# Optimization experiments

Measured on AMD Instinct MI355X. Metric: run time of the kernel, lower is better.

The kernel has to match this reference:

```python
import jax, jax.numpy as jnp
import numpy as np

R = 128            # coarse grid resolution (hash-grid domain)
SCALE = 2          # scale_factor
VS_COARSE = 1.0    # coarse voxel size
VS_FINE = VS_COARSE / SCALE
N_IN = 400_000
C = 32

# 8 trilinear corner offsets, fixed
CORNERS = np.stack(np.meshgrid([0, 1], [0, 1], [0, 1], indexing='ij'), -1).reshape(-1, 3)


def setup_inputs() -> dict:
    key = jax.random.key(0)
    k1, k2 = jax.random.split(key)
    coarse_coords = jax.random.randint(k1, (N_IN, 3), 0, R, dtype=jnp.int32)
    feat = jax.random.normal(k2, (N_IN, C), dtype=jnp.float32)
    # fine grid = subdivided coarse grid: each coarse voxel -> SCALE^3 children
    offs = jnp.stack(
        jnp.meshgrid(jnp.arange(SCALE), jnp.arange(SCALE), jnp.arange(SCALE), indexing='ij'),
        -1).reshape(-1, 3).astype(jnp.int32)  # [8,3]
    fine_coords = (coarse_coords[:, None, :] * SCALE + offs[None]).reshape(-1, 3)  # [8*N_IN,3]
    return {"feat": feat, "coarse_coords": coarse_coords, "fine_coords": fine_coords}


def reference(feat, coarse_coords, fine_coords):
    """Trilinear upsample: sample coarse sparse-voxel features at fine voxel centers.
    Emulates in_grid.sample_trilinear(out_grid.grid_to_world(active_coords), feat).
    Hash-grid lookup is emulated with a dense index volume; missing neighbors
    contribute zero feature (standard sparse-grid convention).
    """
    n_in = feat.shape[0]
    # build coord -> row index volume (stand-in for the voxel hash map)
    table = -jnp.ones((R, R, R), jnp.int32)
    table = table.at[coarse_coords[:, 0], coarse_coords[:, 1], coarse_coords[:, 2]].set(
        jnp.arange(n_in, dtype=jnp.int32))
    # fine voxel centers in world space (centers at (ijk+0.5)*voxel_size)
    out_pos = (fine_coords.astype(jnp.float32) + 0.5) * VS_FINE          # [M,3]
    # continuous coarse-grid coords; coarse centers at (i+0.5)*VS_COARSE
    g = out_pos / VS_COARSE - 0.5                                        # [M,3]
    base = jnp.floor(g)
    frac = g - base                                                      # [M,3]
    corners = jnp.asarray(CORNERS, jnp.int32)                            # [8,3]
    cc = base.astype(jnp.int32)[:, None, :] + corners[None]              # [M,8,3]
    inb = jnp.all((cc >= 0) & (cc < R), axis=-1)                         # [M,8]
    ccc = jnp.clip(cc, 0, R - 1)
    idx = table[ccc[..., 0], ccc[..., 1], ccc[..., 2]]                   # [M,8]
    valid = inb & (idx >= 0)
    # trilinear weights: prod over xyz of frac or (1-frac)
    w3 = jnp.where(corners[None].astype(jnp.float32) > 0,
                   frac[:, None, :], 1.0 - frac[:, None, :])             # [M,8,3]
    w = jnp.prod(w3, axis=-1) * valid.astype(jnp.float32)                # [M,8]
    f = feat[jnp.clip(idx, 0, n_in - 1)]                                 # [M,8,C]
    return jnp.einsum('mk,mkc->mc', w, f)                                # [M,C]
```

## Files before the change

kernel.cpp:

```cpp
#include <hip/hip_runtime.h>


#define R 128
#define TABLE_ELEMS (R * R * R)

typedef float f32x4 __attribute__((ext_vector_type(4)));

__global__ void build_table_kernel(const int* __restrict__ coarse,
                                   int* __restrict__ table, int n) {
    int i = blockIdx.x * blockDim.x + threadIdx.x;
    if (i >= n) return;
    int x = coarse[i * 3 + 0];
    int y = coarse[i * 3 + 1];
    int z = coarse[i * 3 + 2];
    atomicMax(&table[(x * R + y) * R + z], i);
}

__global__ void __launch_bounds__(256)
upsample_kernel(const f32x4* __restrict__ feat4,
                const int* __restrict__ coarse,
                const int* __restrict__ table,
                f32x4* __restrict__ out4,
                int n_in) {
    __shared__ f32x4 sm[4][27 * 8];

    int wib  = threadIdx.x >> 6;
    int lane = threadIdx.x & 63;
    int vi   = blockIdx.x * 4 + wib;
    vi = __builtin_amdgcn_readfirstlane(vi);
    if (vi >= n_in) return;

    int cx = coarse[vi * 3 + 0];
    int cy = coarse[vi * 3 + 1];
    int cz = coarse[vi * 3 + 2];

    int myidx = -1;
    if (lane < 27) {
        int dx  = lane / 9;
        int rem = lane - dx * 9;
        int dy  = rem / 3;
        int dz  = rem - dy * 3;
        int x = cx + dx - 1, y = cy + dy - 1, z = cz + dz - 1;
        if ((unsigned)x < (unsigned)R && (unsigned)y < (unsigned)R &&
            (unsigned)z < (unsigned)R)
            myidx = table[(x * R + y) * R + z];
    }
    unsigned long long vmask = __ballot(myidx >= 0);

    int g = lane >> 3;
    int part = lane & 7;
    f32x4* smw = sm[wib];
#pragma unroll
    for (int r = 0; r < 4; ++r) {
        int nb  = r * 8 + g;
        int idx = __shfl(myidx, nb);
        if (idx >= 0)
            smw[nb * 8 + part] = feat4[(size_t)idx * 8 + part];
    }
    asm volatile("s_waitcnt lgkmcnt(0)" ::: "memory");
    __builtin_amdgcn_sched_barrier(0);

    int ox = (g >> 2) & 1, oy = (g >> 1) & 1, oz = g & 1;
    float wx0 = 0.25f + 0.5f * (float)ox, wx1 = 0.75f - 0.5f * (float)ox;
    float wy0 = 0.25f + 0.5f * (float)oy, wy1 = 0.75f - 0.5f * (float)oy;
    float wz0 = 0.25f + 0.5f * (float)oz, wz1 = 0.75f - 0.5f * (float)oz;

    f32x4 acc = (f32x4)(0.f);
#pragma unroll
    for (int k = 0; k < 8; ++k) {
        int kx = (k >> 2) & 1, ky = (k >> 1) & 1, kz = k & 1;
        int nb = (ox + kx) * 9 + (oy + ky) * 3 + (oz + kz);
        if ((vmask >> nb) & 1ull) {
            float w = (kx ? wx1 : wx0) * (ky ? wy1 : wy0) * (kz ? wz1 : wz0);
            f32x4 f = smw[nb * 8 + part];
            acc += w * f;
        }
    }

    __builtin_nontemporal_store(acc, &out4[(size_t)vi * 64 + lane]);
}

extern "C" void kernel_launch(void* const* d_in, const int* in_sizes, int n_in_arrs,
                              void* d_out, int out_size, void* d_ws, size_t ws_size,
                              hipStream_t stream) {
    const float* feat = (const float*)d_in[0];
    const int* coarse = (const int*)d_in[1];

    int n_in = in_sizes[1] / 3;
    int* table = (int*)d_ws;

    hipMemsetAsync(table, 0xFF, (size_t)TABLE_ELEMS * sizeof(int), stream);

    build_table_kernel<<<(n_in + 255) / 256, 256, 0, stream>>>(coarse, table, n_in);

    int nblocks = (n_in + 3) / 4;
    upsample_kernel<<<nblocks, 256, 0, stream>>>(
        (const f32x4*)feat, coarse, table, (f32x4*)d_out, n_in);
}
```

Baseline: 580.7 us.

## Reorder voxel processing by spatial 8^3 bucket for gather locality

Adds a counting sort of coarse voxels into 4096 spatial buckets (count, single-block scan, atomic scatter) and has the upsample kernel process voxels in that permuted order. Neighbouring waves then touch nearby table entries and shared neighbour features, which is meant to improve cache hit rates on the random gathers. The cost is two extra kernel launches, contended atomics on bucket counters, and output writes that become scattered rather than sequential.

```diff
diff --git a/kernel.cpp b/kernel.cpp
--- a/kernel.cpp
+++ b/kernel.cpp
@@ -3,32 +3,77 @@
 
 #define R 128
 #define TABLE_ELEMS (R * R * R)
+#define NBUCKET 4096
 
 typedef float f32x4 __attribute__((ext_vector_type(4)));
 
+__device__ __forceinline__ int bucket_of(int x, int y, int z) {
+    return ((x >> 3) << 8) | ((y >> 3) << 4) | (z >> 3);
+}
+
 __global__ void build_table_kernel(const int* __restrict__ coarse,
-                                   int* __restrict__ table, int n) {
+                                   int* __restrict__ table,
+                                   int* __restrict__ counts, int n) {
     int i = blockIdx.x * blockDim.x + threadIdx.x;
     if (i >= n) return;
     int x = coarse[i * 3 + 0];
     int y = coarse[i * 3 + 1];
     int z = coarse[i * 3 + 2];
     atomicMax(&table[(x * R + y) * R + z], i);
+    atomicAdd(&counts[bucket_of(x, y, z)], 1);
+}
+
+__global__ void __launch_bounds__(256)
+scan_kernel(const int* __restrict__ counts, int* __restrict__ offs) {
+    __shared__ int part[256];
+    int t = threadIdx.x;
+    int local[16];
+    int s = 0;
+#pragma unroll
+    for (int k = 0; k < 16; ++k) {
+        local[k] = s;
+        s += counts[t * 16 + k];
+    }
+    part[t] = s;
+    __syncthreads();
+    for (int d = 1; d < 256; d <<= 1) {
+        int v = (t >= d) ? part[t - d] : 0;
+        __syncthreads();
+        part[t] += v;
+        __syncthreads();
+    }
+    int base = (t == 0) ? 0 : part[t - 1];
+#pragma unroll
+    for (int k = 0; k < 16; ++k) offs[t * 16 + k] = base + local[k];
+}
+
+__global__ void scatter_kernel(const int* __restrict__ coarse,
+                               int* __restrict__ offs,
+                               int* __restrict__ perm, int n) {
+    int i = blockIdx.x * blockDim.x + threadIdx.x;
+    if (i >= n) return;
+    int x = coarse[i * 3 + 0];
+    int y = coarse[i * 3 + 1];
+    int z = coarse[i * 3 + 2];
+    int pos = atomicAdd(&offs[bucket_of(x, y, z)], 1);
+    perm[pos] = i;
 }
 
 __global__ void __launch_bounds__(256)
 upsample_kernel(const f32x4* __restrict__ feat4,
                 const int* __restrict__ coarse,
                 const int* __restrict__ table,
+                const int* __restrict__ perm,
                 f32x4* __restrict__ out4,
                 int n_in) {
     __shared__ f32x4 sm[4][27 * 8];
 
     int wib  = threadIdx.x >> 6;
     int lane = threadIdx.x & 63;
-    int vi   = blockIdx.x * 4 + wib;
+    int wid  = blockIdx.x * 4 + wib;
+    if (wid >= n_in) return;
+    int vi = perm[wid];
     vi = __builtin_amdgcn_readfirstlane(vi);
-    if (vi >= n_in) return;
 
     int cx = coarse[vi * 3 + 0];
     int cy = coarse[vi * 3 + 1];
@@ -87,13 +132,21 @@
     const int* coarse = (const int*)d_in[1];
 
     int n_in = in_sizes[1] / 3;
-    int* table = (int*)d_ws;
+
+    int* table  = (int*)d_ws;
+    int* counts = table + TABLE_ELEMS;
+    int* offs   = counts + NBUCKET;
+    int* perm   = offs + NBUCKET;
 
     hipMemsetAsync(table, 0xFF, (size_t)TABLE_ELEMS * sizeof(int), stream);
+    hipMemsetAsync(counts, 0x00, (size_t)NBUCKET * sizeof(int), stream);
 
-    build_table_kernel<<<(n_in + 255) / 256, 256, 0, stream>>>(coarse, table, n_in);
+    int nb256 = (n_in + 255) / 256;
+    build_table_kernel<<<nb256, 256, 0, stream>>>(coarse, table, counts, n_in);
+    scan_kernel<<<1, 256, 0, stream>>>(counts, offs);
+    scatter_kernel<<<nb256, 256, 0, stream>>>(coarse, offs, perm, n_in);
 
     int nblocks = (n_in + 3) / 4;
     upsample_kernel<<<nblocks, 256, 0, stream>>>(
-        (const f32x4*)feat, coarse, table, (f32x4*)d_out, n_in);
+        (const f32x4*)feat, coarse, table, perm, (f32x4*)d_out, n_in);
 }
```

Result: slower. 689.4 us (+18.7%).

## Make upsample kernel persistent with software-pipelined table probes and feature gathers

Applied to the files above, without the earlier changes.

Replaces one-wave-per-voxel launch with a persistent grid of 1792 blocks where each wave loops over voxels with a stride. The table probe is issued two iterations ahead and the neighbor feature gathers one iteration ahead, held in registers, so global-memory latency overlaps the LDS store, the interpolation and the output store. This removes launch and wave-startup overhead and exposes memory-level parallelism per wave, at the cost of more registers (launch bounds now request 7 blocks per CU) and no explicit barrier between writing and reading the per-wave LDS slot across iterations.

```diff
diff --git a/kernel.cpp b/kernel.cpp
--- a/kernel.cpp
+++ b/kernel.cpp
@@ -16,68 +16,100 @@
     atomicMax(&table[(x * R + y) * R + z], i);
 }
 
-__global__ void __launch_bounds__(256)
+__global__ void __launch_bounds__(256, 7)
 upsample_kernel(const f32x4* __restrict__ feat4,
                 const int* __restrict__ coarse,
                 const int* __restrict__ table,
                 f32x4* __restrict__ out4,
-                int n_in) {
+                int n_in, int nw) {
     __shared__ f32x4 sm[4][27 * 8];
 
     int wib  = threadIdx.x >> 6;
     int lane = threadIdx.x & 63;
-    int vi   = blockIdx.x * 4 + wib;
-    vi = __builtin_amdgcn_readfirstlane(vi);
-    if (vi >= n_in) return;
+    int wid  = __builtin_amdgcn_readfirstlane(blockIdx.x * 4 + wib);
+    f32x4* smw = sm[wib];
 
-    int cx = coarse[vi * 3 + 0];
-    int cy = coarse[vi * 3 + 1];
-    int cz = coarse[vi * 3 + 2];
+    int g    = lane >> 3;
+    int part = lane & 7;
 
-    int myidx = -1;
-    if (lane < 27) {
-        int dx  = lane / 9;
-        int rem = lane - dx * 9;
-        int dy  = rem / 3;
-        int dz  = rem - dy * 3;
-        int x = cx + dx - 1, y = cy + dy - 1, z = cz + dz - 1;
-        if ((unsigned)x < (unsigned)R && (unsigned)y < (unsigned)R &&
-            (unsigned)z < (unsigned)R)
-            myidx = table[(x * R + y) * R + z];
-    }
-    unsigned long long vmask = __ballot(myidx >= 0);
-
-    int g = lane >> 3;
-    int part = lane & 7;
-    f32x4* smw = sm[wib];
-#pragma unroll
-    for (int r = 0; r < 4; ++r) {
-        int nb  = r * 8 + g;
-        int idx = __shfl(myidx, nb);
-        if (idx >= 0)
-            smw[nb * 8 + part] = feat4[(size_t)idx * 8 + part];
-    }
-    asm volatile("s_waitcnt lgkmcnt(0)" ::: "memory");
-    __builtin_amdgcn_sched_barrier(0);
+    int dx   = lane / 9;
+    int prem = lane - dx * 9;
+    int dy   = prem / 3;
+    int dz   = prem - dy * 3;
+    bool isprobe = lane < 27;
 
     int ox = (g >> 2) & 1, oy = (g >> 1) & 1, oz = g & 1;
     float wx0 = 0.25f + 0.5f * (float)ox, wx1 = 0.75f - 0.5f * (float)ox;
     float wy0 = 0.25f + 0.5f * (float)oy, wy1 = 0.75f - 0.5f * (float)oy;
     float wz0 = 0.25f + 0.5f * (float)oz, wz1 = 0.75f - 0.5f * (float)oz;
 
-    f32x4 acc = (f32x4)(0.f);
+    auto probe = [&](int vi) -> int {
+        int idx = -1;
+        if (vi < n_in && isprobe) {
+            int cx = coarse[vi * 3 + 0];
+            int cy = coarse[vi * 3 + 1];
+            int cz = coarse[vi * 3 + 2];
+            int x = cx + dx - 1, y = cy + dy - 1, z = cz + dz - 1;
+            if ((unsigned)x < (unsigned)R && (unsigned)y < (unsigned)R &&
+                (unsigned)z < (unsigned)R)
+                idx = table[(x * R + y) * R + z];
+        }
+        return idx;
+    };
+
+    int vi = wid;
+    int m_cur = probe(vi);
+    unsigned long long vmask = __ballot(m_cur >= 0);
+    int i0 = __shfl(m_cur, g);
+    int i1 = __shfl(m_cur, 8 + g);
+    int i2 = __shfl(m_cur, 16 + g);
+    int i3 = __shfl(m_cur, 24 + g);
+    f32x4 f0, f1, f2, f3;
+    if (i0 >= 0) f0 = feat4[(size_t)i0 * 8 + part];
+    if (i1 >= 0) f1 = feat4[(size_t)i1 * 8 + part];
+    if (i2 >= 0) f2 = feat4[(size_t)i2 * 8 + part];
+    if (i3 >= 0) f3 = feat4[(size_t)i3 * 8 + part];
+    int m_nxt = probe(vi + nw);
+
+    while (vi < n_in) {
+        if (i0 >= 0) smw[(g)      * 8 + part] = f0;
+        if (i1 >= 0) smw[(8 + g)  * 8 + part] = f1;
+        if (i2 >= 0) smw[(16 + g) * 8 + part] = f2;
+        if (i3 >= 0) smw[(24 + g) * 8 + part] = f3;
+
+        unsigned long long vmask_n = __ballot(m_nxt >= 0);
+        int n0 = __shfl(m_nxt, g);
+        int n1 = __shfl(m_nxt, 8 + g);
+        int n2 = __shfl(m_nxt, 16 + g);
+        int n3 = __shfl(m_nxt, 24 + g);
+        f32x4 nf0, nf1, nf2, nf3;
+        if (n0 >= 0) nf0 = feat4[(size_t)n0 * 8 + part];
+        if (n1 >= 0) nf1 = feat4[(size_t)n1 * 8 + part];
+        if (n2 >= 0) nf2 = feat4[(size_t)n2 * 8 + part];
+        if (n3 >= 0) nf3 = feat4[(size_t)n3 * 8 + part];
+
+        int m_nn = probe(vi + 2 * nw);
+
+        asm volatile("s_waitcnt lgkmcnt(0)" ::: "memory");
+        __builtin_amdgcn_sched_barrier(0);
+        f32x4 acc = (f32x4)(0.f);
 #pragma unroll
-    for (int k = 0; k < 8; ++k) {
-        int kx = (k >> 2) & 1, ky = (k >> 1) & 1, kz = k & 1;
-        int nb = (ox + kx) * 9 + (oy + ky) * 3 + (oz + kz);
-        if ((vmask >> nb) & 1ull) {
-            float w = (kx ? wx1 : wx0) * (ky ? wy1 : wy0) * (kz ? wz1 : wz0);
-            f32x4 f = smw[nb * 8 + part];
-            acc += w * f;
+        for (int k = 0; k < 8; ++k) {
+            int kx = (k >> 2) & 1, ky = (k >> 1) & 1, kz = k & 1;
+            int nb = (ox + kx) * 9 + (oy + ky) * 3 + (oz + kz);
+            if ((vmask >> nb) & 1ull) {
+                float w = (kx ? wx1 : wx0) * (ky ? wy1 : wy0) * (kz ? wz1 : wz0);
+                acc += w * smw[nb * 8 + part];
+            }
         }
+        __builtin_nontemporal_store(acc, &out4[(size_t)vi * 64 + lane]);
+
+        vi += nw;
+        vmask = vmask_n;
+        i0 = n0; i1 = n1; i2 = n2; i3 = n3;
+        f0 = nf0; f1 = nf1; f2 = nf2; f3 = nf3;
+        m_nxt = m_nn;
     }
-
-    __builtin_nontemporal_store(acc, &out4[(size_t)vi * 64 + lane]);
 }
 
 extern "C" void kernel_launch(void* const* d_in, const int* in_sizes, int n_in_arrs,
@@ -93,7 +125,11 @@
 
     build_table_kernel<<<(n_in + 255) / 256, 256, 0, stream>>>(coarse, table, n_in);
 
-    int nblocks = (n_in + 3) / 4;
+    int nblocks = 1792;
+    int max_needed = (n_in + 3) / 4;
+    if (nblocks > max_needed) nblocks = max_needed;
+    int nw = nblocks * 4;
+
     upsample_kernel<<<nblocks, 256, 0, stream>>>(
-        (const f32x4*)feat, coarse, table, (f32x4*)d_out, n_in);
+        (const f32x4*)feat, coarse, table, (f32x4*)d_out, n_in, nw);
 }
```

New measurement: 908.4 us. 56.4% more time.

## Process two coarse voxels per wave and gather neighbors via direct global-to-LDS loads

Applied to the files above, without the earlier changes.

Each wavefront now handles two coarse voxels, one per 32-lane half doing the 27-neighbor table lookup, which halves the block count. Neighbor feature rows are fetched with global_load_lds so the data goes straight to LDS without passing through VGPRs, and the wait becomes vmcnt. This aims to cut per-wave overhead and register round-trips on the gather, at the cost of twice the LDS per wave and a more complex mask and indexing scheme.

```diff
diff --git a/kernel.cpp b/kernel.cpp
--- a/kernel.cpp
+++ b/kernel.cpp
@@ -16,28 +16,37 @@
     atomicMax(&table[(x * R + y) * R + z], i);
 }
 
+__device__ __forceinline__ void gload_lds16(const f32x4* g, f32x4* l) {
+    __builtin_amdgcn_global_load_lds(
+        (const __attribute__((address_space(1))) void*)g,
+        (__attribute__((address_space(3))) void*)l, 16, 0, 0);
+}
+
 __global__ void __launch_bounds__(256)
 upsample_kernel(const f32x4* __restrict__ feat4,
                 const int* __restrict__ coarse,
                 const int* __restrict__ table,
                 f32x4* __restrict__ out4,
                 int n_in) {
-    __shared__ f32x4 sm[4][27 * 8];
+    __shared__ f32x4 sm[4][2][256];
 
     int wib  = threadIdx.x >> 6;
     int lane = threadIdx.x & 63;
-    int vi   = blockIdx.x * 4 + wib;
-    vi = __builtin_amdgcn_readfirstlane(vi);
-    if (vi >= n_in) return;
+    int half = lane >> 5;
+    int pl   = lane & 31;
 
-    int cx = coarse[vi * 3 + 0];
-    int cy = coarse[vi * 3 + 1];
-    int cz = coarse[vi * 3 + 2];
+    int viA = __builtin_amdgcn_readfirstlane(blockIdx.x * 8 + wib * 2);
+    if (viA >= n_in) return;
+    int viB = viA + 1;
 
+    int vi_p = half ? viB : viA;
     int myidx = -1;
-    if (lane < 27) {
-        int dx  = lane / 9;
-        int rem = lane - dx * 9;
+    if (pl < 27 && vi_p < n_in) {
+        int cx = coarse[vi_p * 3 + 0];
+        int cy = coarse[vi_p * 3 + 1];
+        int cz = coarse[vi_p * 3 + 2];
+        int dx  = pl / 9;
+        int rem = pl - dx * 9;
         int dy  = rem / 3;
         int dz  = rem - dy * 3;
         int x = cx + dx - 1, y = cy + dy - 1, z = cz + dz - 1;
@@ -46,18 +55,26 @@
             myidx = table[(x * R + y) * R + z];
     }
     unsigned long long vmask = __ballot(myidx >= 0);
+    unsigned maskA = (unsigned)(vmask & 0x7FFFFFFull);
+    unsigned maskB = (unsigned)((vmask >> 32) & 0x7FFFFFFull);
 
-    int g = lane >> 3;
+    int g    = lane >> 3;
     int part = lane & 7;
-    f32x4* smw = sm[wib];
+    f32x4* smA = &sm[wib][0][0];
+    f32x4* smB = &sm[wib][1][0];
 #pragma unroll
     for (int r = 0; r < 4; ++r) {
-        int nb  = r * 8 + g;
-        int idx = __shfl(myidx, nb);
+        int idx = __shfl(myidx, r * 8 + g);
         if (idx >= 0)
-            smw[nb * 8 + part] = feat4[(size_t)idx * 8 + part];
+            gload_lds16(&feat4[(size_t)idx * 8 + part], smA + r * 64);
     }
-    asm volatile("s_waitcnt lgkmcnt(0)" ::: "memory");
+#pragma unroll
+    for (int r = 0; r < 4; ++r) {
+        int idx = __shfl(myidx, 32 + r * 8 + g);
+        if (idx >= 0)
+            gload_lds16(&feat4[(size_t)idx * 8 + part], smB + r * 64);
+    }
+    asm volatile("s_waitcnt vmcnt(0)" ::: "memory");
     __builtin_amdgcn_sched_barrier(0);
 
     int ox = (g >> 2) & 1, oy = (g >> 1) & 1, oz = g & 1;
@@ -65,19 +82,20 @@
     float wy0 = 0.25f + 0.5f * (float)oy, wy1 = 0.75f - 0.5f * (float)oy;
     float wz0 = 0.25f + 0.5f * (float)oz, wz1 = 0.75f - 0.5f * (float)oz;
 
-    f32x4 acc = (f32x4)(0.f);
+    f32x4 accA = (f32x4)(0.f);
+    f32x4 accB = (f32x4)(0.f);
 #pragma unroll
     for (int k = 0; k < 8; ++k) {
         int kx = (k >> 2) & 1, ky = (k >> 1) & 1, kz = k & 1;
         int nb = (ox + kx) * 9 + (oy + ky) * 3 + (oz + kz);
-        if ((vmask >> nb) & 1ull) {
-            float w = (kx ? wx1 : wx0) * (ky ? wy1 : wy0) * (kz ? wz1 : wz0);
-            f32x4 f = smw[nb * 8 + part];
-            acc += w * f;
-        }
+        float w = (kx ? wx1 : wx0) * (ky ? wy1 : wy0) * (kz ? wz1 : wz0);
+        if ((maskA >> nb) & 1u) accA += w * smA[nb * 8 + part];
+        if ((maskB >> nb) & 1u) accB += w * smB[nb * 8 + part];
     }
 
-    __builtin_nontemporal_store(acc, &out4[(size_t)vi * 64 + lane]);
+    __builtin_nontemporal_store(accA, &out4[(size_t)viA * 64 + lane]);
+    if (viB < n_in)
+        __builtin_nontemporal_store(accB, &out4[(size_t)viB * 64 + lane]);
 }
 
 extern "C" void kernel_launch(void* const* d_in, const int* in_sizes, int n_in_arrs,
@@ -93,7 +111,7 @@
 
     build_table_kernel<<<(n_in + 255) / 256, 256, 0, stream>>>(coarse, table, n_in);
 
-    int nblocks = (n_in + 3) / 4;
+    int nblocks = (n_in + 7) / 8;
     upsample_kernel<<<nblocks, 256, 0, stream>>>(
         (const f32x4*)feat, coarse, table, (f32x4*)d_out, n_in);
 }
```

Measured after the change: 567.5 us. 2.3% less time.
